# Kernel optimization log

Measured on AMD Instinct MI355X. Metric: run time of the kernel, lower is better.

The kernel has to match this reference:

```python
import jax, jax.numpy as jnp
import numpy as np

N_NODES, N_EDGES, N_GRAPHS = 50000, 800000, 64
F_NODE, F_EDGE, F_GLOB, F_MSG, F_OUT, HID = 64, 64, 64, 64, 128, 32


def setup_inputs() -> dict:
    key = jax.random.key(0)
    ks = jax.random.split(key, 16)
    s = lambda fan_in: 1.0 / np.sqrt(fan_in)
    inp = {
        "x": jax.random.normal(ks[0], (N_NODES, F_NODE), dtype=jnp.float32),
        "edge_index": jax.random.randint(ks[1], (2, N_EDGES), 0, N_NODES),
        "edge_attr": jax.random.normal(ks[2], (N_EDGES, F_EDGE), dtype=jnp.float32),
        "u": jax.random.normal(ks[3], (N_GRAPHS, F_GLOB), dtype=jnp.float32),
        "batch": jnp.sort(jax.random.randint(ks[4], (N_NODES,), 0, N_GRAPHS)),
        # node_mlp_1: Lin(2*F_NODE+F_EDGE, 32) -> ReLU -> Lin(32, F_MSG) -> ReLU
        "W1": jax.random.normal(ks[5], (2 * F_NODE + F_EDGE, HID), dtype=jnp.float32) * s(2 * F_NODE + F_EDGE),
        "b1": jnp.zeros((HID,), jnp.float32),
        "W2": jax.random.normal(ks[6], (HID, F_MSG), dtype=jnp.float32) * s(HID),
        "b2": jnp.zeros((F_MSG,), jnp.float32),
        # node_mlp_2: Lin(2*F_MSG+F_NODE+F_GLOB, 32) -> ReLU -> Lin(32, F_OUT) -> ReLU
        "W3": jax.random.normal(ks[7], (2 * F_MSG + F_NODE + F_GLOB, HID), dtype=jnp.float32) * s(2 * F_MSG + F_NODE + F_GLOB),
        "b3": jnp.zeros((HID,), jnp.float32),
        "W4": jax.random.normal(ks[8], (HID, F_OUT), dtype=jnp.float32) * s(HID),
        "b4": jnp.zeros((F_OUT,), jnp.float32),
    }
    return inp


def reference(x, edge_index, edge_attr, u, batch, W1, b1, W2, b2, W3, b3, W4, b4):
    N = x.shape[0]
    row, col = edge_index[0], edge_index[1]
    # edge MLP (dropout off / eval mode)
    m = jnp.concatenate([x[row], x[col], edge_attr], axis=1)  # [E, 2F+Fe]
    m = jax.nn.relu(m @ W1 + b1)
    m = jax.nn.relu(m @ W2 + b2)  # [E, F_MSG]
    # scatter-mean and scatter-max onto destination nodes (col)
    cnt = jax.ops.segment_sum(jnp.ones((col.shape[0], 1), m.dtype), col, num_segments=N)  # [N,1]
    agg_mean = jax.ops.segment_sum(m, col, num_segments=N) / jnp.maximum(cnt, 1.0)
    agg_max = jax.ops.segment_max(m, col, num_segments=N)
    agg_max = jnp.where(cnt > 0, agg_max, 0.0)  # empty segments -> 0 (torch_scatter convention)
    # node MLP
    h = jnp.concatenate([x, agg_mean, agg_max, u[batch]], axis=1)
    h = jax.nn.relu(h @ W3 + b3)
    return jax.nn.relu(h @ W4 + b4)
```

## Files before the change

kernel.cpp:

```cpp
#include <hip/hip_runtime.h>
#include <hip/hip_bf16.h>
#include <stdint.h>

constexpr int FN   = 64;
constexpr int HIDN = 32;
constexpr int FMSG = 64;
constexpr int FOUT = 128;

using short8 = __attribute__((ext_vector_type(8))) short;
using f32x4  = __attribute__((ext_vector_type(4))) float;

union Frag { short8 v; uint32_t u[4]; };

__device__ __forceinline__ uint32_t packrn(float a, float b) {
    union { __hip_bfloat162 h; uint32_t u; } cv;
    cv.h = __float22bfloat162_rn(make_float2(a, b));
    return cv.u;
}
__device__ __forceinline__ float bf16_to_f(uint32_t h16) {
    return __uint_as_float(h16 << 16);
}

__device__ __forceinline__ int node_of(const int* __restrict__ offs, int N, int target) {
    int l = 0, r = N + 1;
    while (l + 1 < r) {
        const int m = (l + r) >> 1;
        if (offs[m] <= target) l = m; else r = m;
    }
    return l;
}

__global__ __launch_bounds__(256) void zero_cnt_kernel(int* __restrict__ cnt, int N)
{
    const int i = blockIdx.x * 256 + threadIdx.x;
    if (i < N) cnt[i] = 0;
}

__global__ __launch_bounds__(256) void mega_prep_kernel(
    const int* __restrict__ ei, int* __restrict__ cnt, int* __restrict__ rank,
    const float* __restrict__ x, const float* __restrict__ u,
    const float* __restrict__ W1, const float* __restrict__ b1,
    const float* __restrict__ W2,
    const float* __restrict__ W3, const float* __restrict__ b3,
    const float* __restrict__ W4,
    float* __restrict__ Pa, float* __restrict__ Pb, float* __restrict__ Qc,
    float* __restrict__ Qu,
    uint32_t* __restrict__ PW1, uint32_t* __restrict__ PW2,
    uint32_t* __restrict__ PW3, uint32_t* __restrict__ PW4,
    uint4* __restrict__ zbase, size_t zquads,
    int E, int N, int G, int BH, int BPN, int BZ)
{
    __shared__ float xs_all[4 * 64 * 33];
    const int b   = blockIdx.x;
    const int tid = threadIdx.x;

    if (b < BH) {
        const int base = (b * 256 + tid) * 8;
        if (base + 8 <= E) {
            const int4 c0 = *reinterpret_cast<const int4*>(ei + E + base);
            const int4 c1 = *reinterpret_cast<const int4*>(ei + E + base + 4);
            int4 r0, r1;
            r0.x = atomicAdd(cnt + c0.x, 1);
            r0.y = atomicAdd(cnt + c0.y, 1);
            r0.z = atomicAdd(cnt + c0.z, 1);
            r0.w = atomicAdd(cnt + c0.w, 1);
            r1.x = atomicAdd(cnt + c1.x, 1);
            r1.y = atomicAdd(cnt + c1.y, 1);
            r1.z = atomicAdd(cnt + c1.z, 1);
            r1.w = atomicAdd(cnt + c1.w, 1);
            *reinterpret_cast<int4*>(rank + base)     = r0;
            *reinterpret_cast<int4*>(rank + base + 4) = r1;
        } else {
            for (int e = base; e < E; ++e) rank[e] = atomicAdd(cnt + ei[E + e], 1);
        }
        return;
    }
    if (b < BH + BPN) {
        const int w    = tid >> 6;
        const int lane = tid & 63;
        float* xs = xs_all + w * (64 * 33);
        const int nbase = (b - BH) * 256 + w * 64;
        if (nbase >= N) return;

        float a[HIDN], bq[HIDN], cc[HIDN];
#pragma unroll
        for (int j = 0; j < HIDN; ++j) { a[j] = b1[j]; bq[j] = 0.0f; cc[j] = b3[j]; }

#pragma unroll
        for (int c = 0; c < 2; ++c) {
#pragma unroll
            for (int i = 0; i < 8; ++i) {
                const int idx = i * 64 + lane;
                const int row = idx >> 3, cq = idx & 7;
                const int nr  = min(nbase + row, N - 1);
                const float4 v = *reinterpret_cast<const float4*>(
                    x + (size_t)nr * FN + c * 32 + cq * 4);
                float* d = xs + row * 33 + cq * 4;
                d[0] = v.x; d[1] = v.y; d[2] = v.z; d[3] = v.w;
            }
            const float* xr = xs + lane * 33;
#pragma unroll 2
            for (int k = 0; k < 32; k += 4) {
                const float v0 = xr[k], v1 = xr[k + 1], v2 = xr[k + 2], v3 = xr[k + 3];
                const int kg = c * 32 + k;
                const float* wa = W1 + kg * HIDN;
                const float* wb = W1 + FN * HIDN + kg * HIDN;
                const float* wc = W3 + kg * HIDN;
#pragma unroll
                for (int j = 0; j < HIDN; ++j) {
                    float aj = a[j], bj = bq[j], cj = cc[j];
                    aj = fmaf(v0, wa[j], aj);            bj = fmaf(v0, wb[j], bj);            cj = fmaf(v0, wc[j], cj);
                    aj = fmaf(v1, wa[HIDN + j], aj);     bj = fmaf(v1, wb[HIDN + j], bj);     cj = fmaf(v1, wc[HIDN + j], cj);
                    aj = fmaf(v2, wa[2 * HIDN + j], aj); bj = fmaf(v2, wb[2 * HIDN + j], bj); cj = fmaf(v2, wc[2 * HIDN + j], cj);
                    aj = fmaf(v3, wa[3 * HIDN + j], aj); bj = fmaf(v3, wb[3 * HIDN + j], bj); cj = fmaf(v3, wc[3 * HIDN + j], cj);
                    a[j] = aj; bq[j] = bj; cc[j] = cj;
                }
            }
        }
        const int n = nbase + lane;
        if (n >= N) return;
        float4* pa = reinterpret_cast<float4*>(Pa + (size_t)n * HIDN);
        float4* pb = reinterpret_cast<float4*>(Pb + (size_t)n * HIDN);
        float4* qc = reinterpret_cast<float4*>(Qc + (size_t)n * HIDN);
#pragma unroll
        for (int q = 0; q < HIDN / 4; ++q) {
            pa[q] = make_float4(a[4*q], a[4*q+1], a[4*q+2], a[4*q+3]);
            pb[q] = make_float4(bq[4*q], bq[4*q+1], bq[4*q+2], bq[4*q+3]);
            qc[q] = make_float4(cc[4*q], cc[4*q+1], cc[4*q+2], cc[4*q+3]);
        }
        return;
    }
    if (b == BH + BPN) {
        const float* WC = W1 + 2 * FN * HIDN;
        for (int i = tid; i < 2048; i += 256) {
            const int j = i >> 6, k2 = i & 63;
            uint32_t v;
            if (k2 < 32) {
                v = packrn(WC[(2 * k2) * HIDN + j], WC[(2 * k2 + 1) * HIDN + j]);
            } else if (k2 < 48) {
                const int r0 = 2 * (k2 - 32);
                v = packrn(r0 == j ? 1.0f : 0.0f, r0 + 1 == j ? 1.0f : 0.0f);
            } else {
                const int r0 = 2 * (k2 - 48);
                v = packrn(r0 == j ? 1.0f : 0.0f, r0 + 1 == j ? 1.0f : 0.0f);
            }
            PW1[i] = v;
        }
        for (int i = tid; i < 1024; i += 256) {
            const int j = i >> 4, k2 = i & 15;
            PW2[i] = packrn(W2[(2 * k2) * FMSG + j], W2[(2 * k2 + 1) * FMSG + j]);
        }
        const float* W3m = W3 + 64 * HIDN;
        for (int i = tid; i < 3072; i += 256) {
            const int j = i / 96, k2 = i - j * 96;
            uint32_t v;
            if (k2 < 64) {
                v = packrn(W3m[(2 * k2) * HIDN + j], W3m[(2 * k2 + 1) * HIDN + j]);
            } else if (k2 < 80) {
                const int r0 = 2 * (k2 - 64);
                v = packrn(r0 == j ? 1.0f : 0.0f, r0 + 1 == j ? 1.0f : 0.0f);
            } else {
                const int r0 = 2 * (k2 - 80);
                v = packrn(r0 == j ? 1.0f : 0.0f, r0 + 1 == j ? 1.0f : 0.0f);
            }
            PW3[i] = v;
        }
        for (int i = tid; i < 2048; i += 256) {
            const int j = i >> 4, k2 = i & 15;
            PW4[i] = packrn(W4[(2 * k2) * FOUT + j], W4[(2 * k2 + 1) * FOUT + j]);
        }
        const float* W3u = W3 + 192 * HIDN;
        for (int i = tid; i < G * HIDN; i += 256) {
            const int g = i >> 5, j = i & 31;
            const float* ur = u + (size_t)g * FN;
            float acc = 0.0f;
#pragma unroll 8
            for (int k = 0; k < FN; ++k) acc = fmaf(ur[k], W3u[k * HIDN + j], acc);
            Qu[i] = acc;
        }
        return;
    }
    const size_t stride = (size_t)BZ * 256;
    const uint4 z = make_uint4(0u, 0u, 0u, 0u);
    for (size_t i = (size_t)(b - BH - BPN - 1) * 256 + tid; i < zquads; i += stride)
        zbase[i] = z;
}

__global__ __launch_bounds__(256) void scanA_kernel(
    const int* __restrict__ cnt, int* __restrict__ part, int N)
{
    __shared__ int red[256];
    const int tid  = threadIdx.x;
    const int base = blockIdx.x * 2048 + tid * 8;
    int s = 0;
    if (base + 8 <= N) {
        const int4 a = *reinterpret_cast<const int4*>(cnt + base);
        const int4 b = *reinterpret_cast<const int4*>(cnt + base + 4);
        s = a.x + a.y + a.z + a.w + b.x + b.y + b.z + b.w;
    } else {
        for (int i = base; i < min(base + 8, N); ++i) s += cnt[i];
    }
    red[tid] = s;
    __syncthreads();
    for (int d = 128; d > 0; d >>= 1) {
        if (tid < d) red[tid] += red[tid + d];
        __syncthreads();
    }
    if (tid == 0) part[blockIdx.x] = red[0];
}

__global__ __launch_bounds__(256) void scanC_kernel(
    const int* __restrict__ cnt, const int* __restrict__ part,
    int* __restrict__ offs, int NB, int N, int E)
{
    __shared__ int sb[256];
    const int tid  = threadIdx.x;
    int px = 0;
    for (int i = 0; i < (int)blockIdx.x; ++i) px += part[i];

    const int base = blockIdx.x * 2048 + tid * 8;
    int v[8];
    int tsum = 0;
#pragma unroll
    for (int q = 0; q < 8; ++q) {
        const int i = base + q;
        v[q] = (i < N) ? cnt[i] : 0;
        tsum += v[q];
    }
    sb[tid] = tsum;
    __syncthreads();
    for (int d = 1; d < 256; d <<= 1) {
        const int t = (tid >= d) ? sb[tid - d] : 0;
        __syncthreads();
        sb[tid] += t;
        __syncthreads();
    }
    int run = px + sb[tid] - tsum;
#pragma unroll
    for (int q = 0; q < 8; ++q) {
        const int i = base + q;
        if (i < N) offs[i] = run;
        run += v[q];
    }
    if (blockIdx.x == 0 && tid == 0) offs[N] = E;
}

__global__ __launch_bounds__(256) void scatter_ntile_kernel(
    const int* __restrict__ ei, const int* __restrict__ offs,
    const int* __restrict__ rank, int4* __restrict__ re4,
    int2* __restrict__ ntile, int E, int N, int NT, int SB)
{
    const int tid = threadIdx.x;
    if ((int)blockIdx.x < SB) {
        const int e = blockIdx.x * 256 + tid;
        if (e >= E) return;
        const int row = ei[e];
        const int col = ei[E + e];
        const int pos = offs[col] + rank[e];
        re4[pos] = make_int4(row, col, e, 0);
    } else {
        const int t = ((int)blockIdx.x - SB) * 256 + tid;
        if (t >= NT) return;
        const int a = node_of(offs, N, t * 64);
        const int b = node_of(offs, N, min(t * 64 + 63, E - 1));
        ntile[t] = make_int2(a, b);
    }
}

__global__ __launch_bounds__(128) void fused_edge_mfma(
    const float* __restrict__ ea,
    const uint32_t* __restrict__ PW1, const uint32_t* __restrict__ PW2,
    const float* __restrict__ b2,
    const float* __restrict__ Pa, const float* __restrict__ Pb,
    const int4* __restrict__ re4, const int* __restrict__ offs,
    const int2* __restrict__ ntile,
    float* __restrict__ agg_sum, int* __restrict__ agg_maxb,
    int N, int E, int NT)
{
    __shared__ uint32_t smem_all[2 * 64 * 34];
    const int w    = threadIdx.x >> 6;
    const int t    = blockIdx.x * 2 + w;
    if (t >= NT) return;
    uint32_t* smem = smem_all + w * (64 * 34);
    const int lane = threadIdx.x & 63;
    const int l15  = lane & 15;
    const int l4   = lane >> 4;
    const int e0   = t * 64;
    const int e1   = min(e0 + 64, E);
    const int2 nrange = ntile[t];

    const int p = e0 + lane;
    const int4 rce = re4[min(p, E - 1)];

    int er[4], rr[4], cr[4];
#pragma unroll
    for (int mt = 0; mt < 4; ++mt) {
        er[mt] = __shfl(rce.z, mt * 16 + l15, 64);
        rr[mt] = __shfl(rce.x, mt * 16 + l15, 64);
        cr[mt] = __shfl(rce.y, mt * 16 + l15, 64);
    }

    f32x4 acc1[4][2];
#pragma unroll
    for (int mt = 0; mt < 4; ++mt)
#pragma unroll
        for (int nt = 0; nt < 2; ++nt)
            acc1[mt][nt] = (f32x4){0.f, 0.f, 0.f, 0.f};

    float4 raw[4][2][2];
#pragma unroll
    for (int mt = 0; mt < 4; ++mt)
#pragma unroll
        for (int ks = 0; ks < 2; ++ks) {
            const float* src = ea + (size_t)er[mt] * FN + ks * 32 + l4 * 8;
            raw[mt][ks][0] = *reinterpret_cast<const float4*>(src);
            raw[mt][ks][1] = *reinterpret_cast<const float4*>(src + 4);
        }
#pragma unroll
    for (int ks = 0; ks < 2; ++ks) {
        Frag Bk[2];
#pragma unroll
        for (int nt = 0; nt < 2; ++nt) {
            const uint4 q = *reinterpret_cast<const uint4*>(
                &PW1[(nt * 16 + l15) * 64 + ks * 16 + l4 * 4]);
            Bk[nt].u[0] = q.x; Bk[nt].u[1] = q.y;
            Bk[nt].u[2] = q.z; Bk[nt].u[3] = q.w;
        }
        Frag A[4];
#pragma unroll
        for (int mt = 0; mt < 4; ++mt) {
            const float4 f0 = raw[mt][ks][0], f1 = raw[mt][ks][1];
            A[mt].u[0] = packrn(f0.x, f0.y);
            A[mt].u[1] = packrn(f0.z, f0.w);
            A[mt].u[2] = packrn(f1.x, f1.y);
            A[mt].u[3] = packrn(f1.z, f1.w);
        }
#pragma unroll
        for (int mt = 0; mt < 4; ++mt)
#pragma unroll
            for (int nt = 0; nt < 2; ++nt)
                acc1[mt][nt] = __builtin_amdgcn_mfma_f32_16x16x32_bf16(
                    A[mt].v, Bk[nt].v, acc1[mt][nt], 0, 0, 0);
    }
#pragma unroll
    for (int mt = 0; mt < 4; ++mt) {
        const float* sa = Pa + (size_t)rr[mt] * HIDN + l4 * 8;
        const float* sb = Pb + (size_t)cr[mt] * HIDN + l4 * 8;
        raw[mt][0][0] = *reinterpret_cast<const float4*>(sa);
        raw[mt][0][1] = *reinterpret_cast<const float4*>(sa + 4);
        raw[mt][1][0] = *reinterpret_cast<const float4*>(sb);
        raw[mt][1][1] = *reinterpret_cast<const float4*>(sb + 4);
    }
#pragma unroll
    for (int ks = 2; ks < 4; ++ks) {
        Frag Bk[2];
#pragma unroll
        for (int nt = 0; nt < 2; ++nt) {
            const uint4 q = *reinterpret_cast<const uint4*>(
                &PW1[(nt * 16 + l15) * 64 + ks * 16 + l4 * 4]);
            Bk[nt].u[0] = q.x; Bk[nt].u[1] = q.y;
            Bk[nt].u[2] = q.z; Bk[nt].u[3] = q.w;
        }
        Frag A[4];
#pragma unroll
        for (int mt = 0; mt < 4; ++mt) {
            const float4 f0 = raw[mt][ks - 2][0], f1 = raw[mt][ks - 2][1];
            A[mt].u[0] = packrn(f0.x, f0.y);
            A[mt].u[1] = packrn(f0.z, f0.w);
            A[mt].u[2] = packrn(f1.x, f1.y);
            A[mt].u[3] = packrn(f1.z, f1.w);
        }
#pragma unroll
        for (int mt = 0; mt < 4; ++mt)
#pragma unroll
            for (int nt = 0; nt < 2; ++nt)
                acc1[mt][nt] = __builtin_amdgcn_mfma_f32_16x16x32_bf16(
                    A[mt].v, Bk[nt].v, acc1[mt][nt], 0, 0, 0);
    }

    float* Hl = reinterpret_cast<float*>(smem);
#pragma unroll
    for (int mt = 0; mt < 4; ++mt)
#pragma unroll
        for (int nt = 0; nt < 2; ++nt)
#pragma unroll
            for (int r = 0; r < 4; ++r) {
                const int et = mt * 16 + l4 * 4 + r;
                Hl[et * 34 + nt * 16 + l15] = fmaxf(acc1[mt][nt][r], 0.0f);
            }

    Frag A2[4];
#pragma unroll
    for (int mt = 0; mt < 4; ++mt) {
        const float* hb = &Hl[(mt * 16 + l15) * 34 + l4 * 8];
        const float2 g0 = *reinterpret_cast<const float2*>(hb + 0);
        const float2 g1 = *reinterpret_cast<const float2*>(hb + 2);
        const float2 g2 = *reinterpret_cast<const float2*>(hb + 4);
        const float2 g3 = *reinterpret_cast<const float2*>(hb + 6);
        A2[mt].u[0] = packrn(g0.x, g0.y);
        A2[mt].u[1] = packrn(g1.x, g1.y);
        A2[mt].u[2] = packrn(g2.x, g2.y);
        A2[mt].u[3] = packrn(g3.x, g3.y);
    }

    Frag B2f[4];
#pragma unroll
    for (int nt = 0; nt < 4; ++nt) {
        const uint4 q = *reinterpret_cast<const uint4*>(
            &PW2[(nt * 16 + l15) * 16 + l4 * 4]);
        B2f[nt].u[0] = q.x; B2f[nt].u[1] = q.y;
        B2f[nt].u[2] = q.z; B2f[nt].u[3] = q.w;
    }

#pragma unroll
    for (int nt = 0; nt < 4; ++nt) {
        const float b2v = b2[nt * 16 + l15];
        f32x4 a2c[4];
#pragma unroll
        for (int mt = 0; mt < 4; ++mt) {
            a2c[mt] = (f32x4){0.f, 0.f, 0.f, 0.f};
            a2c[mt] = __builtin_amdgcn_mfma_f32_16x16x32_bf16(
                A2[mt].v, B2f[nt].v, a2c[mt], 0, 0, 0);
        }
        const int j = nt * 16 + l15;
#pragma unroll
        for (int mt = 0; mt < 4; ++mt)
#pragma unroll
            for (int rp2 = 0; rp2 < 2; ++rp2) {
                const int q2 = mt * 8 + l4 * 2 + rp2;
                const float v0 = fmaxf(a2c[mt][rp2 * 2]     + b2v, 0.0f);
                const float v1 = fmaxf(a2c[mt][rp2 * 2 + 1] + b2v, 0.0f);
                smem[q2 * 64 + (j ^ (((q2 >> 1) & 1) << 4))] = packrn(v0, v1);
            }
    }

    const int n0 = nrange.x, n1 = nrange.y;
    for (int n = n0; n <= n1; ++n) {
        const int s0 = offs[n], t0 = offs[n + 1];
        const int sl = max(s0, e0) - e0, tl = min(t0, e1) - e0;
        float sum = 0.0f, mx = 0.0f;
        int q = sl;
        if (q < tl && (q & 1)) {
            const int q2 = q >> 1;
            const uint32_t wv = smem[q2 * 64 + (lane ^ (((q2 >> 1) & 1) << 4))];
            const float v = bf16_to_f(wv >> 16);
            sum += v; mx = fmaxf(mx, v); ++q;
        }
        for (; q + 1 < tl; q += 2) {
            const int q2 = q >> 1;
            const uint32_t wv = smem[q2 * 64 + (lane ^ (((q2 >> 1) & 1) << 4))];
            const float v0 = bf16_to_f(wv & 0xffffu), v1 = bf16_to_f(wv >> 16);
            sum += v0 + v1; mx = fmaxf(mx, fmaxf(v0, v1));
        }
        if (q < tl) {
            const int q2 = q >> 1;
            const uint32_t wv = smem[q2 * 64 + (lane ^ (((q2 >> 1) & 1) << 4))];
            const float v = bf16_to_f(wv & 0xffffu);
            sum += v; mx = fmaxf(mx, v);
        }
        float* sp = agg_sum  + (size_t)n * FMSG + lane;
        int*   mp = agg_maxb + (size_t)n * FMSG + lane;
        if (s0 >= e0 && t0 <= e1) {
            *sp = sum;
            *mp = __float_as_int(mx);
        } else {
            unsafeAtomicAdd(sp, sum);
            atomicMax(mp, __float_as_int(mx));
        }
    }
}

__global__ __launch_bounds__(256) void node_mfma(
    const float* __restrict__ Qc, const float* __restrict__ Qu,
    const int*   __restrict__ batch,
    const uint32_t* __restrict__ PW3, const uint32_t* __restrict__ PW4,
    const float* __restrict__ b4,
    const float* __restrict__ agg_sum, const int* __restrict__ agg_maxb,
    const int*   __restrict__ offs,
    float* __restrict__ out, int N)
{
    __shared__ float Hl_all[4 * 32 * 34];
    const int w    = threadIdx.x >> 6;
    float* Hl      = Hl_all + w * (32 * 34);
    const int lane = threadIdx.x & 63;
    const int l15  = lane & 15;
    const int l4   = lane >> 4;
    const int n0   = blockIdx.x * 128 + w * 32;
    if (n0 >= N) return;

    int   arn[2], gb[2];
    float ainv[2];
#pragma unroll
    for (int mt = 0; mt < 2; ++mt) {
        arn[mt] = min(n0 + mt * 16 + l15, N - 1);
        const int deg = offs[arn[mt] + 1] - offs[arn[mt]];
        ainv[mt] = (deg > 0) ? 1.0f / (float)deg : 0.0f;
        gb[mt]  = batch[arn[mt]];
    }

    f32x4 acc1[2][2];
#pragma unroll
    for (int mt = 0; mt < 2; ++mt)
#pragma unroll
        for (int nt = 0; nt < 2; ++nt)
            acc1[mt][nt] = (f32x4){0.f, 0.f, 0.f, 0.f};

#pragma unroll
    for (int ks = 0; ks < 6; ++ks) {
        Frag Bk[2];
#pragma unroll
        for (int nt = 0; nt < 2; ++nt) {
            const uint4 q = *reinterpret_cast<const uint4*>(
                &PW3[(nt * 16 + l15) * 96 + ks * 16 + l4 * 4]);
            Bk[nt].u[0] = q.x; Bk[nt].u[1] = q.y;
            Bk[nt].u[2] = q.z; Bk[nt].u[3] = q.w;
        }
        Frag A[2];
        if (ks < 2) {
#pragma unroll
            for (int mt = 0; mt < 2; ++mt) {
                const float4* gp = reinterpret_cast<const float4*>(
                    agg_sum + (size_t)arn[mt] * FMSG + ks * 32 + l4 * 8);
                const float4 f0 = gp[0], f1 = gp[1];
                const float s = ainv[mt];
                A[mt].u[0] = packrn(f0.x * s, f0.y * s);
                A[mt].u[1] = packrn(f0.z * s, f0.w * s);
                A[mt].u[2] = packrn(f1.x * s, f1.y * s);
                A[mt].u[3] = packrn(f1.z * s, f1.w * s);
            }
        } else if (ks < 4) {
#pragma unroll
            for (int mt = 0; mt < 2; ++mt) {
                const uint4* gp = reinterpret_cast<const uint4*>(
                    agg_maxb + (size_t)arn[mt] * FMSG + (ks - 2) * 32 + l4 * 8);
                const uint4 u0 = gp[0], u1 = gp[1];
                A[mt].u[0] = packrn(__uint_as_float(u0.x), __uint_as_float(u0.y));
                A[mt].u[1] = packrn(__uint_as_float(u0.z), __uint_as_float(u0.w));
                A[mt].u[2] = packrn(__uint_as_float(u1.x), __uint_as_float(u1.y));
                A[mt].u[3] = packrn(__uint_as_float(u1.z), __uint_as_float(u1.w));
            }
        } else {
#pragma unroll
            for (int mt = 0; mt < 2; ++mt) {
                const float* src = (ks == 4)
                    ? Qc + (size_t)arn[mt] * HIDN + l4 * 8
                    : Qu + (size_t)gb[mt]  * HIDN + l4 * 8;
                const float4 f0 = *reinterpret_cast<const float4*>(src);
                const float4 f1 = *reinterpret_cast<const float4*>(src + 4);
                A[mt].u[0] = packrn(f0.x, f0.y);
                A[mt].u[1] = packrn(f0.z, f0.w);
                A[mt].u[2] = packrn(f1.x, f1.y);
                A[mt].u[3] = packrn(f1.z, f1.w);
            }
        }
#pragma unroll
        for (int mt = 0; mt < 2; ++mt)
#pragma unroll
            for (int nt = 0; nt < 2; ++nt)
                acc1[mt][nt] = __builtin_amdgcn_mfma_f32_16x16x32_bf16(
                    A[mt].v, Bk[nt].v, acc1[mt][nt], 0, 0, 0);
    }

#pragma unroll
    for (int mt = 0; mt < 2; ++mt)
#pragma unroll
        for (int nt = 0; nt < 2; ++nt)
#pragma unroll
            for (int r = 0; r < 4; ++r) {
                const int rw = mt * 16 + l4 * 4 + r;
                Hl[rw * 34 + nt * 16 + l15] = fmaxf(acc1[mt][nt][r], 0.0f);
            }

    Frag A2[2];
#pragma unroll
    for (int mt = 0; mt < 2; ++mt) {
        const float* hb = &Hl[(mt * 16 + l15) * 34 + l4 * 8];
        const float2 g0 = *reinterpret_cast<const float2*>(hb + 0);
        const float2 g1 = *reinterpret_cast<const float2*>(hb + 2);
        const float2 g2 = *reinterpret_cast<const float2*>(hb + 4);
        const float2 g3 = *reinterpret_cast<const float2*>(hb + 6);
        A2[mt].u[0] = packrn(g0.x, g0.y);
        A2[mt].u[1] = packrn(g1.x, g1.y);
        A2[mt].u[2] = packrn(g2.x, g2.y);
        A2[mt].u[3] = packrn(g3.x, g3.y);
    }

#pragma unroll
    for (int nt = 0; nt < 8; ++nt) {
        Frag B4f;
        const uint4 q = *reinterpret_cast<const uint4*>(
            &PW4[(nt * 16 + l15) * 16 + l4 * 4]);
        B4f.u[0] = q.x; B4f.u[1] = q.y; B4f.u[2] = q.z; B4f.u[3] = q.w;
        const float b4v = b4[nt * 16 + l15];
        f32x4 tacc[2];
#pragma unroll
        for (int mt = 0; mt < 2; ++mt) {
            tacc[mt] = (f32x4){0.f, 0.f, 0.f, 0.f};
            tacc[mt] = __builtin_amdgcn_mfma_f32_16x16x32_bf16(
                A2[mt].v, B4f.v, tacc[mt], 0, 0, 0);
        }
#pragma unroll
        for (int mt = 0; mt < 2; ++mt)
#pragma unroll
            for (int r = 0; r < 4; ++r) {
                const int node = n0 + mt * 16 + l4 * 4 + r;
                if (node < N)
                    out[(size_t)node * FOUT + nt * 16 + l15] =
                        fmaxf(tacc[mt][r] + b4v, 0.0f);
            }
    }
}

extern "C" void kernel_launch(void* const* d_in, const int* in_sizes, int n_in,
                              void* d_out, int out_size, void* d_ws, size_t ws_size,
                              hipStream_t stream)
{
    const float* x     = (const float*)d_in[0];
    const int*   ei    = (const int*)  d_in[1];
    const float* ea    = (const float*)d_in[2];
    const float* u     = (const float*)d_in[3];
    const int*   batch = (const int*)  d_in[4];
    const float* W1    = (const float*)d_in[5];
    const float* b1    = (const float*)d_in[6];
    const float* W2    = (const float*)d_in[7];
    const float* b2    = (const float*)d_in[8];
    const float* W3    = (const float*)d_in[9];
    const float* b3    = (const float*)d_in[10];
    const float* W4    = (const float*)d_in[11];
    const float* b4    = (const float*)d_in[12];
    float* out = (float*)d_out;

    const int N = in_sizes[0] / FN;
    const int E = in_sizes[1] / 2;
    const int G = in_sizes[3] / FN;
    const int NT = (E + 63) / 64;

    char* wp = (char*)d_ws;
    auto take = [&](size_t bytes) -> void* {
        void* r = (void*)wp;
        wp += (bytes + 255) & ~(size_t)255;
        return r;
    };
    float*    agg_sum  = (float*)   take((size_t)N * FMSG * 4);
    int*      agg_maxb = (int*)     take((size_t)N * FMSG * 4);
    char*     zero_end = wp;
    int*      cnt      = (int*)     take((size_t)N * 4);
    int*      offs     = (int*)     take(((size_t)N + 1) * 4);
    int*      rank     = (int*)     take((size_t)E * 4);
    int4*     re4      = (int4*)    take((size_t)E * 16);
    int2*     ntile    = (int2*)    take((size_t)NT * 8);
    float*    Pa       = (float*)   take((size_t)N * HIDN * 4);
    float*    Pb       = (float*)   take((size_t)N * HIDN * 4);
    float*    Qc       = (float*)   take((size_t)N * HIDN * 4);
    float*    Qu       = (float*)   take((size_t)G * HIDN * 4);
    uint32_t* PW1      = (uint32_t*)take(2048 * 4);
    uint32_t* PW2      = (uint32_t*)take(1024 * 4);
    uint32_t* PW3      = (uint32_t*)take(3072 * 4);
    uint32_t* PW4      = (uint32_t*)take(2048 * 4);
    int*      part     = (int*)     take(64 * 4);

    const int BH  = (E + 2047) / 2048;
    const int BPN = (N + 255) / 256;
    const int BZ  = 256;
    const int NB  = (N + 2047) / 2048;
    const int SB  = (E + 255) / 256;
    const int TB  = (NT + 255) / 256;
    const size_t zquads = (size_t)(zero_end - (char*)agg_sum) / 16;

    zero_cnt_kernel<<<(N + 255) / 256, 256, 0, stream>>>(cnt, N);
    mega_prep_kernel<<<BH + BPN + 1 + BZ, 256, 0, stream>>>(
        ei, cnt, rank, x, u, W1, b1, W2, W3, b3, W4,
        Pa, Pb, Qc, Qu, PW1, PW2, PW3, PW4,
        (uint4*)agg_sum, zquads, E, N, G, BH, BPN, BZ);
    scanA_kernel   <<<NB, 256, 0, stream>>>(cnt, part, N);
    scanC_kernel   <<<NB, 256, 0, stream>>>(cnt, part, offs, NB, N, E);
    scatter_ntile_kernel<<<SB + TB, 256, 0, stream>>>(
        ei, offs, rank, re4, ntile, E, N, NT, SB);
    fused_edge_mfma<<<(NT + 1) / 2, 128, 0, stream>>>(
        ea, PW1, PW2, b2, Pa, Pb, re4, offs, ntile, agg_sum, agg_maxb, N, E, NT);
    node_mfma      <<<(N + 127) / 128, 256, 0, stream>>>(
        Qc, Qu, batch, PW3, PW4, b4, agg_sum, agg_maxb, offs, out, N);
}
```

Measured before the change: 197.2 us.

## Merge frontend prep kernels into one cooperative kernel with grid syncs

Replaces the five frontend launches (zero count, prep, two scan passes, scatter) with one persistent cooperative kernel that separates phases with grid-wide syncs and work-strided loops. The goal is to remove per-launch overhead and the idle gaps between small dependent kernels. In exchange the grid is capped by occupancy, so the histogram, node-precompute and zeroing phases get fewer blocks with fixed shares (half, quarter, quarter). The kernel also calls host queries for device attributes and occupancy on every invocation, and grid.sync has its own cost. The old multi-kernel path stays as a fallback when cooperative launch is unavailable.

```diff
diff --git a/kernel.cpp b/kernel.cpp
--- a/kernel.cpp
+++ b/kernel.cpp
@@ -1,6 +1,9 @@
 #include <hip/hip_runtime.h>
+#include <hip/hip_cooperative_groups.h>
 #include <hip/hip_bf16.h>
 #include <stdint.h>
+
+namespace cg = cooperative_groups;
 
 constexpr int FN   = 64;
 constexpr int HIDN = 32;
@@ -30,160 +33,282 @@
     return l;
 }
 
+struct FEParams {
+    const int*   ei;
+    int*         cnt;
+    int*         rank;
+    const float* x;
+    const float* u;
+    const float* W1; const float* b1; const float* W2;
+    const float* W3; const float* b3; const float* W4;
+    float* Pa; float* Pb; float* Qc; float* Qu;
+    uint32_t* PW1; uint32_t* PW2; uint32_t* PW3; uint32_t* PW4;
+    uint4* aggz; size_t aggquads;
+    uint4* cntz; int cntquads;
+    int4*  re4;  int2* ntile;
+    int*   offs; int* part;
+    int E, N, G, NB, SB, TB, NT, BH, BPN, GRID;
+};
+
+__device__ void fe_pack_weights(const FEParams& P, int tid)
+{
+    const float* WC = P.W1 + 2 * FN * HIDN;
+    for (int i = tid; i < 2048; i += 256) {
+        const int j = i >> 6, k2 = i & 63;
+        uint32_t v;
+        if (k2 < 32) {
+            v = packrn(WC[(2 * k2) * HIDN + j], WC[(2 * k2 + 1) * HIDN + j]);
+        } else if (k2 < 48) {
+            const int r0 = 2 * (k2 - 32);
+            v = packrn(r0 == j ? 1.0f : 0.0f, r0 + 1 == j ? 1.0f : 0.0f);
+        } else {
+            const int r0 = 2 * (k2 - 48);
+            v = packrn(r0 == j ? 1.0f : 0.0f, r0 + 1 == j ? 1.0f : 0.0f);
+        }
+        P.PW1[i] = v;
+    }
+    for (int i = tid; i < 1024; i += 256) {
+        const int j = i >> 4, k2 = i & 15;
+        P.PW2[i] = packrn(P.W2[(2 * k2) * FMSG + j], P.W2[(2 * k2 + 1) * FMSG + j]);
+    }
+    const float* W3m = P.W3 + 64 * HIDN;
+    for (int i = tid; i < 3072; i += 256) {
+        const int j = i / 96, k2 = i - j * 96;
+        uint32_t v;
+        if (k2 < 64) {
+            v = packrn(W3m[(2 * k2) * HIDN + j], W3m[(2 * k2 + 1) * HIDN + j]);
+        } else if (k2 < 80) {
+            const int r0 = 2 * (k2 - 64);
+            v = packrn(r0 == j ? 1.0f : 0.0f, r0 + 1 == j ? 1.0f : 0.0f);
+        } else {
+            const int r0 = 2 * (k2 - 80);
+            v = packrn(r0 == j ? 1.0f : 0.0f, r0 + 1 == j ? 1.0f : 0.0f);
+        }
+        P.PW3[i] = v;
+    }
+    for (int i = tid; i < 2048; i += 256) {
+        const int j = i >> 4, k2 = i & 15;
+        P.PW4[i] = packrn(P.W4[(2 * k2) * FOUT + j], P.W4[(2 * k2 + 1) * FOUT + j]);
+    }
+    const float* W3u = P.W3 + 192 * HIDN;
+    for (int i = tid; i < P.G * HIDN; i += 256) {
+        const int g = i >> 5, j = i & 31;
+        const float* ur = P.u + (size_t)g * FN;
+        float acc = 0.0f;
+#pragma unroll 8
+        for (int k = 0; k < FN; ++k) acc = fmaf(ur[k], W3u[k * HIDN + j], acc);
+        P.Qu[i] = acc;
+    }
+}
+
+__device__ void fe_hist_chunk(const FEParams& P, int c, int tid)
+{
+    const int base = (c * 256 + tid) * 8;
+    const int E = P.E;
+    if (base + 8 <= E) {
+        const int4 c0 = *reinterpret_cast<const int4*>(P.ei + E + base);
+        const int4 c1 = *reinterpret_cast<const int4*>(P.ei + E + base + 4);
+        int4 r0, r1;
+        r0.x = atomicAdd(P.cnt + c0.x, 1);
+        r0.y = atomicAdd(P.cnt + c0.y, 1);
+        r0.z = atomicAdd(P.cnt + c0.z, 1);
+        r0.w = atomicAdd(P.cnt + c0.w, 1);
+        r1.x = atomicAdd(P.cnt + c1.x, 1);
+        r1.y = atomicAdd(P.cnt + c1.y, 1);
+        r1.z = atomicAdd(P.cnt + c1.z, 1);
+        r1.w = atomicAdd(P.cnt + c1.w, 1);
+        *reinterpret_cast<int4*>(P.rank + base)     = r0;
+        *reinterpret_cast<int4*>(P.rank + base + 4) = r1;
+    } else {
+        for (int e = base; e < E; ++e) P.rank[e] = atomicAdd(P.cnt + P.ei[E + e], 1);
+    }
+}
+
+__device__ void fe_node_pre(const FEParams& P, int unit, int tid, float* xs_all)
+{
+    const int w    = tid >> 6;
+    const int lane = tid & 63;
+    float* xs = xs_all + w * (64 * 33);
+    const int nbase = unit * 256 + w * 64;
+    const int N = P.N;
+    if (nbase >= N) return;
+
+    float a[HIDN], bq[HIDN], cc[HIDN];
+#pragma unroll
+    for (int j = 0; j < HIDN; ++j) { a[j] = P.b1[j]; bq[j] = 0.0f; cc[j] = P.b3[j]; }
+
+#pragma unroll
+    for (int c = 0; c < 2; ++c) {
+#pragma unroll
+        for (int i = 0; i < 8; ++i) {
+            const int idx = i * 64 + lane;
+            const int row = idx >> 3, cq = idx & 7;
+            const int nr  = min(nbase + row, N - 1);
+            const float4 v = *reinterpret_cast<const float4*>(
+                P.x + (size_t)nr * FN + c * 32 + cq * 4);
+            float* d = xs + row * 33 + cq * 4;
+            d[0] = v.x; d[1] = v.y; d[2] = v.z; d[3] = v.w;
+        }
+        const float* xr = xs + lane * 33;
+#pragma unroll 2
+        for (int k = 0; k < 32; k += 4) {
+            const float v0 = xr[k], v1 = xr[k + 1], v2 = xr[k + 2], v3 = xr[k + 3];
+            const int kg = c * 32 + k;
+            const float* wa = P.W1 + kg * HIDN;
+            const float* wb = P.W1 + FN * HIDN + kg * HIDN;
+            const float* wc = P.W3 + kg * HIDN;
+#pragma unroll
+            for (int j = 0; j < HIDN; ++j) {
+                float aj = a[j], bj = bq[j], cj = cc[j];
+                aj = fmaf(v0, wa[j], aj);            bj = fmaf(v0, wb[j], bj);            cj = fmaf(v0, wc[j], cj);
+                aj = fmaf(v1, wa[HIDN + j], aj);     bj = fmaf(v1, wb[HIDN + j], bj);     cj = fmaf(v1, wc[HIDN + j], cj);
+                aj = fmaf(v2, wa[2 * HIDN + j], aj); bj = fmaf(v2, wb[2 * HIDN + j], bj); cj = fmaf(v2, wc[2 * HIDN + j], cj);
+                aj = fmaf(v3, wa[3 * HIDN + j], aj); bj = fmaf(v3, wb[3 * HIDN + j], bj); cj = fmaf(v3, wc[3 * HIDN + j], cj);
+                a[j] = aj; bq[j] = bj; cc[j] = cj;
+            }
+        }
+    }
+    const int n = nbase + lane;
+    if (n >= N) return;
+    float4* pa = reinterpret_cast<float4*>(P.Pa + (size_t)n * HIDN);
+    float4* pb = reinterpret_cast<float4*>(P.Pb + (size_t)n * HIDN);
+    float4* qc = reinterpret_cast<float4*>(P.Qc + (size_t)n * HIDN);
+#pragma unroll
+    for (int q = 0; q < HIDN / 4; ++q) {
+        pa[q] = make_float4(a[4*q], a[4*q+1], a[4*q+2], a[4*q+3]);
+        pb[q] = make_float4(bq[4*q], bq[4*q+1], bq[4*q+2], bq[4*q+3]);
+        qc[q] = make_float4(cc[4*q], cc[4*q+1], cc[4*q+2], cc[4*q+3]);
+    }
+}
+
+__global__ __launch_bounds__(256) void frontend_coop(FEParams P)
+{
+    cg::grid_group grid = cg::this_grid();
+    __shared__ __align__(16) char smem_raw[4 * 64 * 33 * 4];
+    const int b   = blockIdx.x;
+    const int tid = threadIdx.x;
+    const int GRID = P.GRID;
+
+    {
+        const uint4 z = make_uint4(0u, 0u, 0u, 0u);
+        for (int i = b * 256 + tid; i < P.cntquads; i += GRID * 256)
+            P.cntz[i] = z;
+        if (b == 0) fe_pack_weights(P, tid);
+    }
+    grid.sync();
+
+    {
+        const int GH = GRID / 2;
+        const int GN = GRID / 4;
+        if (b < GH) {
+            for (int c = b; c < P.BH; c += GH) fe_hist_chunk(P, c, tid);
+        } else if (b < GH + GN) {
+            float* xs_all = reinterpret_cast<float*>(smem_raw);
+            for (int un = b - GH; un < P.BPN; un += GN) fe_node_pre(P, un, tid, xs_all);
+        } else {
+            const int GZ = GRID - GH - GN;
+            const uint4 z = make_uint4(0u, 0u, 0u, 0u);
+            const size_t stride = (size_t)GZ * 256;
+            for (size_t i = (size_t)(b - GH - GN) * 256 + tid; i < P.aggquads; i += stride)
+                P.aggz[i] = z;
+        }
+    }
+    grid.sync();
+
+    if (b < P.NB) {
+        int* red = reinterpret_cast<int*>(smem_raw);
+        const int base = b * 2048 + tid * 8;
+        int s = 0;
+        if (base + 8 <= P.N) {
+            const int4 a0 = *reinterpret_cast<const int4*>(P.cnt + base);
+            const int4 b0 = *reinterpret_cast<const int4*>(P.cnt + base + 4);
+            s = a0.x + a0.y + a0.z + a0.w + b0.x + b0.y + b0.z + b0.w;
+        } else {
+            for (int i = base; i < min(base + 8, P.N); ++i) s += P.cnt[i];
+        }
+        red[tid] = s;
+        __syncthreads();
+        for (int d = 128; d > 0; d >>= 1) {
+            if (tid < d) red[tid] += red[tid + d];
+            __syncthreads();
+        }
+        if (tid == 0) P.part[b] = red[0];
+    }
+    grid.sync();
+
+    if (b < P.NB) {
+        int* sb = reinterpret_cast<int*>(smem_raw);
+        int px = 0;
+        for (int i = 0; i < b; ++i) px += P.part[i];
+        const int base = b * 2048 + tid * 8;
+        int v[8];
+        int tsum = 0;
+#pragma unroll
+        for (int q = 0; q < 8; ++q) {
+            const int i = base + q;
+            v[q] = (i < P.N) ? P.cnt[i] : 0;
+            tsum += v[q];
+        }
+        sb[tid] = tsum;
+        __syncthreads();
+        for (int d = 1; d < 256; d <<= 1) {
+            const int t = (tid >= d) ? sb[tid - d] : 0;
+            __syncthreads();
+            sb[tid] += t;
+            __syncthreads();
+        }
+        int run = px + sb[tid] - tsum;
+#pragma unroll
+        for (int q = 0; q < 8; ++q) {
+            const int i = base + q;
+            if (i < P.N) P.offs[i] = run;
+            run += v[q];
+        }
+        if (b == 0 && tid == 0) P.offs[P.N] = P.E;
+    }
+    grid.sync();
+
+    for (int unit = b; unit < P.SB + P.TB; unit += GRID) {
+        if (unit < P.SB) {
+            const int e = unit * 256 + tid;
+            if (e < P.E) {
+                const int row = P.ei[e];
+                const int col = P.ei[P.E + e];
+                const int pos = P.offs[col] + P.rank[e];
+                P.re4[pos] = make_int4(row, col, e, 0);
+            }
+        } else {
+            const int t = (unit - P.SB) * 256 + tid;
+            if (t < P.NT) {
+                const int a = node_of(P.offs, P.N, t * 64);
+                const int bb = node_of(P.offs, P.N, min(t * 64 + 63, P.E - 1));
+                P.ntile[t] = make_int2(a, bb);
+            }
+        }
+    }
+}
+
 __global__ __launch_bounds__(256) void zero_cnt_kernel(int* __restrict__ cnt, int N)
 {
     const int i = blockIdx.x * 256 + threadIdx.x;
     if (i < N) cnt[i] = 0;
 }
 
-__global__ __launch_bounds__(256) void mega_prep_kernel(
-    const int* __restrict__ ei, int* __restrict__ cnt, int* __restrict__ rank,
-    const float* __restrict__ x, const float* __restrict__ u,
-    const float* __restrict__ W1, const float* __restrict__ b1,
-    const float* __restrict__ W2,
-    const float* __restrict__ W3, const float* __restrict__ b3,
-    const float* __restrict__ W4,
-    float* __restrict__ Pa, float* __restrict__ Pb, float* __restrict__ Qc,
-    float* __restrict__ Qu,
-    uint32_t* __restrict__ PW1, uint32_t* __restrict__ PW2,
-    uint32_t* __restrict__ PW3, uint32_t* __restrict__ PW4,
-    uint4* __restrict__ zbase, size_t zquads,
-    int E, int N, int G, int BH, int BPN, int BZ)
-{
-    __shared__ float xs_all[4 * 64 * 33];
+__global__ __launch_bounds__(256) void mega_prep_kernel(FEParams P, int BZ)
+{
+    __shared__ __align__(16) char smem_raw[4 * 64 * 33 * 4];
     const int b   = blockIdx.x;
     const int tid = threadIdx.x;
-
-    if (b < BH) {
-        const int base = (b * 256 + tid) * 8;
-        if (base + 8 <= E) {
-            const int4 c0 = *reinterpret_cast<const int4*>(ei + E + base);
-            const int4 c1 = *reinterpret_cast<const int4*>(ei + E + base + 4);
-            int4 r0, r1;
-            r0.x = atomicAdd(cnt + c0.x, 1);
-            r0.y = atomicAdd(cnt + c0.y, 1);
-            r0.z = atomicAdd(cnt + c0.z, 1);
-            r0.w = atomicAdd(cnt + c0.w, 1);
-            r1.x = atomicAdd(cnt + c1.x, 1);
-            r1.y = atomicAdd(cnt + c1.y, 1);
-            r1.z = atomicAdd(cnt + c1.z, 1);
-            r1.w = atomicAdd(cnt + c1.w, 1);
-            *reinterpret_cast<int4*>(rank + base)     = r0;
-            *reinterpret_cast<int4*>(rank + base + 4) = r1;
-        } else {
-            for (int e = base; e < E; ++e) rank[e] = atomicAdd(cnt + ei[E + e], 1);
-        }
+    if (b < P.BH) { fe_hist_chunk(P, b, tid); return; }
+    if (b < P.BH + P.BPN) {
+        fe_node_pre(P, b - P.BH, tid, reinterpret_cast<float*>(smem_raw));
         return;
     }
-    if (b < BH + BPN) {
-        const int w    = tid >> 6;
-        const int lane = tid & 63;
-        float* xs = xs_all + w * (64 * 33);
-        const int nbase = (b - BH) * 256 + w * 64;
-        if (nbase >= N) return;
-
-        float a[HIDN], bq[HIDN], cc[HIDN];
-#pragma unroll
-        for (int j = 0; j < HIDN; ++j) { a[j] = b1[j]; bq[j] = 0.0f; cc[j] = b3[j]; }
-
-#pragma unroll
-        for (int c = 0; c < 2; ++c) {
-#pragma unroll
-            for (int i = 0; i < 8; ++i) {
-                const int idx = i * 64 + lane;
-                const int row = idx >> 3, cq = idx & 7;
-                const int nr  = min(nbase + row, N - 1);
-                const float4 v = *reinterpret_cast<const float4*>(
-                    x + (size_t)nr * FN + c * 32 + cq * 4);
-                float* d = xs + row * 33 + cq * 4;
-                d[0] = v.x; d[1] = v.y; d[2] = v.z; d[3] = v.w;
-            }
-            const float* xr = xs + lane * 33;
-#pragma unroll 2
-            for (int k = 0; k < 32; k += 4) {
-                const float v0 = xr[k], v1 = xr[k + 1], v2 = xr[k + 2], v3 = xr[k + 3];
-                const int kg = c * 32 + k;
-                const float* wa = W1 + kg * HIDN;
-                const float* wb = W1 + FN * HIDN + kg * HIDN;
-                const float* wc = W3 + kg * HIDN;
-#pragma unroll
-                for (int j = 0; j < HIDN; ++j) {
-                    float aj = a[j], bj = bq[j], cj = cc[j];
-                    aj = fmaf(v0, wa[j], aj);            bj = fmaf(v0, wb[j], bj);            cj = fmaf(v0, wc[j], cj);
-                    aj = fmaf(v1, wa[HIDN + j], aj);     bj = fmaf(v1, wb[HIDN + j], bj);     cj = fmaf(v1, wc[HIDN + j], cj);
-                    aj = fmaf(v2, wa[2 * HIDN + j], aj); bj = fmaf(v2, wb[2 * HIDN + j], bj); cj = fmaf(v2, wc[2 * HIDN + j], cj);
-                    aj = fmaf(v3, wa[3 * HIDN + j], aj); bj = fmaf(v3, wb[3 * HIDN + j], bj); cj = fmaf(v3, wc[3 * HIDN + j], cj);
-                    a[j] = aj; bq[j] = bj; cc[j] = cj;
-                }
-            }
-        }
-        const int n = nbase + lane;
-        if (n >= N) return;
-        float4* pa = reinterpret_cast<float4*>(Pa + (size_t)n * HIDN);
-        float4* pb = reinterpret_cast<float4*>(Pb + (size_t)n * HIDN);
-        float4* qc = reinterpret_cast<float4*>(Qc + (size_t)n * HIDN);
-#pragma unroll
-        for (int q = 0; q < HIDN / 4; ++q) {
-            pa[q] = make_float4(a[4*q], a[4*q+1], a[4*q+2], a[4*q+3]);
-            pb[q] = make_float4(bq[4*q], bq[4*q+1], bq[4*q+2], bq[4*q+3]);
-            qc[q] = make_float4(cc[4*q], cc[4*q+1], cc[4*q+2], cc[4*q+3]);
-        }
-        return;
-    }
-    if (b == BH + BPN) {
-        const float* WC = W1 + 2 * FN * HIDN;
-        for (int i = tid; i < 2048; i += 256) {
-            const int j = i >> 6, k2 = i & 63;
-            uint32_t v;
-            if (k2 < 32) {
-                v = packrn(WC[(2 * k2) * HIDN + j], WC[(2 * k2 + 1) * HIDN + j]);
-            } else if (k2 < 48) {
-                const int r0 = 2 * (k2 - 32);
-                v = packrn(r0 == j ? 1.0f : 0.0f, r0 + 1 == j ? 1.0f : 0.0f);
-            } else {
-                const int r0 = 2 * (k2 - 48);
-                v = packrn(r0 == j ? 1.0f : 0.0f, r0 + 1 == j ? 1.0f : 0.0f);
-            }
-            PW1[i] = v;
-        }
-        for (int i = tid; i < 1024; i += 256) {
-            const int j = i >> 4, k2 = i & 15;
-            PW2[i] = packrn(W2[(2 * k2) * FMSG + j], W2[(2 * k2 + 1) * FMSG + j]);
-        }
-        const float* W3m = W3 + 64 * HIDN;
-        for (int i = tid; i < 3072; i += 256) {
-            const int j = i / 96, k2 = i - j * 96;
-            uint32_t v;
-            if (k2 < 64) {
-                v = packrn(W3m[(2 * k2) * HIDN + j], W3m[(2 * k2 + 1) * HIDN + j]);
-            } else if (k2 < 80) {
-                const int r0 = 2 * (k2 - 64);
-                v = packrn(r0 == j ? 1.0f : 0.0f, r0 + 1 == j ? 1.0f : 0.0f);
-            } else {
-                const int r0 = 2 * (k2 - 80);
-                v = packrn(r0 == j ? 1.0f : 0.0f, r0 + 1 == j ? 1.0f : 0.0f);
-            }
-            PW3[i] = v;
-        }
-        for (int i = tid; i < 2048; i += 256) {
-            const int j = i >> 4, k2 = i & 15;
-            PW4[i] = packrn(W4[(2 * k2) * FOUT + j], W4[(2 * k2 + 1) * FOUT + j]);
-        }
-        const float* W3u = W3 + 192 * HIDN;
-        for (int i = tid; i < G * HIDN; i += 256) {
-            const int g = i >> 5, j = i & 31;
-            const float* ur = u + (size_t)g * FN;
-            float acc = 0.0f;
-#pragma unroll 8
-            for (int k = 0; k < FN; ++k) acc = fmaf(ur[k], W3u[k * HIDN + j], acc);
-            Qu[i] = acc;
-        }
-        return;
-    }
+    if (b == P.BH + P.BPN) { fe_pack_weights(P, tid); return; }
     const size_t stride = (size_t)BZ * 256;
     const uint4 z = make_uint4(0u, 0u, 0u, 0u);
-    for (size_t i = (size_t)(b - BH - BPN - 1) * 256 + tid; i < zquads; i += stride)
-        zbase[i] = z;
+    for (size_t i = (size_t)(b - P.BH - P.BPN - 1) * 256 + tid; i < P.aggquads; i += stride)
+        P.aggz[i] = z;
 }
 
 __global__ __launch_bounds__(256) void scanA_kernel(
@@ -217,7 +342,6 @@
     const int tid  = threadIdx.x;
     int px = 0;
     for (int i = 0; i < (int)blockIdx.x; ++i) px += part[i];
-
     const int base = blockIdx.x * 2048 + tid * 8;
     int v[8];
     int tsum = 0;
@@ -661,23 +785,50 @@
 
     const int BH  = (E + 2047) / 2048;
     const int BPN = (N + 255) / 256;
-    const int BZ  = 256;
     const int NB  = (N + 2047) / 2048;
     const int SB  = (E + 255) / 256;
     const int TB  = (NT + 255) / 256;
-    const size_t zquads = (size_t)(zero_end - (char*)agg_sum) / 16;
-
-    zero_cnt_kernel<<<(N + 255) / 256, 256, 0, stream>>>(cnt, N);
-    mega_prep_kernel<<<BH + BPN + 1 + BZ, 256, 0, stream>>>(
-        ei, cnt, rank, x, u, W1, b1, W2, W3, b3, W4,
-        Pa, Pb, Qc, Qu, PW1, PW2, PW3, PW4,
-        (uint4*)agg_sum, zquads, E, N, G, BH, BPN, BZ);
-    scanA_kernel   <<<NB, 256, 0, stream>>>(cnt, part, N);
-    scanC_kernel   <<<NB, 256, 0, stream>>>(cnt, part, offs, NB, N, E);
-    scatter_ntile_kernel<<<SB + TB, 256, 0, stream>>>(
-        ei, offs, rank, re4, ntile, E, N, NT, SB);
+    const size_t aggquads = (size_t)(zero_end - (char*)agg_sum) / 16;
+    const int cntquads = N / 4 + ((N & 3) ? 1 : 0);
+
+    FEParams P;
+    P.ei = ei; P.cnt = cnt; P.rank = rank;
+    P.x = x; P.u = u;
+    P.W1 = W1; P.b1 = b1; P.W2 = W2; P.W3 = W3; P.b3 = b3; P.W4 = W4;
+    P.Pa = Pa; P.Pb = Pb; P.Qc = Qc; P.Qu = Qu;
+    P.PW1 = PW1; P.PW2 = PW2; P.PW3 = PW3; P.PW4 = PW4;
+    P.aggz = (uint4*)agg_sum; P.aggquads = aggquads;
+    P.cntz = (uint4*)cnt;     P.cntquads = cntquads;
+    P.re4 = re4; P.ntile = ntile; P.offs = offs; P.part = part;
+    P.E = E; P.N = N; P.G = G; P.NB = NB; P.SB = SB; P.TB = TB; P.NT = NT;
+    P.BH = BH; P.BPN = BPN; P.GRID = 0;
+
+    int coop = 0;
+    hipDeviceGetAttribute(&coop, hipDeviceAttributeCooperativeLaunch, 0);
+    int blocksPerCU = 0;
+    hipOccupancyMaxActiveBlocksPerMultiprocessor(&blocksPerCU, frontend_coop, 256, 0);
+    hipDeviceProp_t prop;
+    hipGetDeviceProperties(&prop, 0);
+    int GRID = blocksPerCU * prop.multiProcessorCount;
+    if (GRID > 2048) GRID = 2048;
+
+    if (coop && GRID >= NB && GRID >= 4) {
+        P.GRID = GRID;
+        void* args[] = { &P };
+        hipLaunchCooperativeKernel(frontend_coop, dim3(GRID), dim3(256),
+                                   args, 0, stream);
+    } else {
+        const int BZ = 256;
+        zero_cnt_kernel<<<(N + 255) / 256, 256, 0, stream>>>(cnt, N);
+        mega_prep_kernel<<<BH + BPN + 1 + BZ, 256, 0, stream>>>(P, BZ);
+        scanA_kernel<<<NB, 256, 0, stream>>>(cnt, part, N);
+        scanC_kernel<<<NB, 256, 0, stream>>>(cnt, part, offs, NB, N, E);
+        scatter_ntile_kernel<<<SB + TB, 256, 0, stream>>>(
+            ei, offs, rank, re4, ntile, E, N, NT, SB);
+    }
+
     fused_edge_mfma<<<(NT + 1) / 2, 128, 0, stream>>>(
         ea, PW1, PW2, b2, Pa, Pb, re4, offs, ntile, agg_sum, agg_maxb, N, E, NT);
-    node_mfma      <<<(N + 127) / 128, 256, 0, stream>>>(
+    node_mfma<<<(N + 127) / 128, 256, 0, stream>>>(
         Qc, Qu, batch, PW3, PW4, b4, agg_sum, agg_maxb, offs, out, N);
 }
```

Result: slower. 264.7 us (+34.3%).
